# Performance work log

Measured on AMD Instinct MI355X. Metric: run time of the kernel, lower is better.

## Reference

```python
import jax, jax.numpy as jnp
import numpy as np

N = 80000      # points
H = 32         # neighbors per point
K = 15         # kernel points (torch-points3d default)
CIN = 128
COUT = 256
D2 = COUT // 4  # 64
INFL = 0.4      # point_influence = prev_grid_size * sigma
KP_RADIUS = 1.5 * INFL  # torch-points3d kernel radius
EPS = 1e-5
SLOPE = 0.2


def setup_inputs() -> dict:
    key = jax.random.key(0)
    ks = jax.random.split(key, 12)
    feats = jax.random.normal(ks[0], (N, CIN), jnp.float32)
    xyz = jax.random.uniform(ks[1], (N, 3), dtype=jnp.float32)
    batch = jnp.zeros((N,), jnp.int32)
    neighbor_idx = jax.random.randint(ks[2], (N, H), 0, N)
    # unary_1: Linear(CIN, D2, bias=False) + BN params
    W1 = jax.random.normal(ks[3], (CIN, D2), jnp.float32) / np.float32(np.sqrt(CIN))
    g1 = jnp.ones((D2,), jnp.float32); b1 = jnp.zeros((D2,), jnp.float32)
    # fixed kernel points inside ball of radius KP_RADIUS (buffer, not trained)
    kdir = jax.random.normal(ks[4], (K, 3), jnp.float32)
    kdir = kdir / jnp.linalg.norm(kdir, axis=1, keepdims=True)
    kp_points = kdir * jax.random.uniform(ks[5], (K, 1), dtype=jnp.float32) * KP_RADIUS
    # per-kernel-point weight matrices [K, D2, D2]
    kp_weights = jax.random.normal(ks[6], (K, D2, D2), jnp.float32) / np.float32(np.sqrt(K * D2))
    # unary_2: Linear(D2, COUT, bias=False) + BN params
    W2 = jax.random.normal(ks[7], (D2, COUT), jnp.float32) / np.float32(np.sqrt(D2))
    g2 = jnp.ones((COUT,), jnp.float32); b2 = jnp.zeros((COUT,), jnp.float32)
    # shortcut: Linear(CIN, COUT, bias=False) + BN params
    Wsc = jax.random.normal(ks[8], (CIN, COUT), jnp.float32) / np.float32(np.sqrt(CIN))
    gsc = jnp.ones((COUT,), jnp.float32); bsc = jnp.zeros((COUT,), jnp.float32)
    return {"feats": feats, "xyz": xyz, "batch": batch, "neighbor_idx": neighbor_idx,
            "W1": W1, "g1": g1, "b1": b1, "kp_points": kp_points, "kp_weights": kp_weights,
            "W2": W2, "g2": g2, "b2": b2, "Wsc": Wsc, "gsc": gsc, "bsc": bsc}


def _bn(x, g, b):
    # FastBatchNorm1d training-mode forward on [N, C]: biased batch stats
    m = jnp.mean(x, axis=0)
    v = jnp.var(x, axis=0)
    return (x - m) * jax.lax.rsqrt(v + EPS) * g + b


def _act(x):
    return jax.nn.leaky_relu(x, SLOPE)


def reference(feats, xyz, batch, neighbor_idx, W1, g1, b1, kp_points, kp_weights,
              W2, g2, b2, Wsc, gsc, bsc):
    # unary_1
    x = _act(_bn(feats @ W1, g1, b1))              # [N, D2]
    # KPConv: gather neighbors, kernel-point linear influence, weighted aggregation
    neighbors = xyz[neighbor_idx] - xyz[:, None, :]            # [N, H, 3]
    diff = neighbors[:, :, None, :] - kp_points[None, None]    # [N, H, K, 3]
    sq = jnp.sum(diff * diff, axis=-1)                          # [N, H, K]
    w = jnp.maximum(1.0 - jnp.sqrt(sq) / INFL, 0.0)             # linear influence
    nx = x[neighbor_idx]                                        # [N, H, D2]
    fk = jnp.einsum('nhk,nhd->nkd', w, nx)                      # [N, K, D2]
    x = jnp.einsum('nkd,kde->ne', fk, kp_weights)               # [N, D2]
    # unary_2
    x = _act(_bn(x @ W2, g2, b2))                               # [N, COUT]
    # shortcut (in_channels != out_channels -> Linear + BN)
    shortcut = _bn(feats @ Wsc, gsc, bsc)                       # [N, COUT]
    return x + shortcut
```

## Files before the change

kernel.cpp:

```cpp
#include <hip/hip_runtime.h>
#include <math.h>

#define NPTS 80000
#define NBH 32
#define KP 15
#define CIN 128
#define COUT 256
#define D2 64
#define INFL 0.4f
#define EPS 1e-5f
#define SLOPE 0.2f

typedef __attribute__((ext_vector_type(8))) short short8;
typedef __attribute__((ext_vector_type(4))) float f32x4;

__device__ inline ushort f2b(float x) {
  unsigned u = __float_as_uint(x);
  return (ushort)((u + 0x7FFFu + ((u >> 16) & 1u)) >> 16);
}
__device__ inline float b2f(ushort v) { return __uint_as_float(((unsigned)v) << 16); }

__global__ __launch_bounds__(256) void k_prep(const float* __restrict__ feats,
                                              const float* __restrict__ W1,
                                              const float* __restrict__ W2,
                                              const float* __restrict__ Wsc,
                                              const float* __restrict__ kw,
                                              ushort* __restrict__ featsb,
                                              ushort* __restrict__ w1s,
                                              ushort* __restrict__ w2s,
                                              ushort* __restrict__ wscs,
                                              ushort* __restrict__ kws) {
  const int NF4 = NPTS * CIN / 4;
  const int TOT = NF4 + 118784;
  int stride = gridDim.x * 256;
  for (int i = blockIdx.x * 256 + threadIdx.x; i < TOT; i += stride) {
    if (i < NF4) {
      float4 v = reinterpret_cast<const float4*>(feats)[i];
      ushort4 o;
      o.x = f2b(v.x); o.y = f2b(v.y); o.z = f2b(v.z); o.w = f2b(v.w);
      reinterpret_cast<ushort4*>(featsb)[i] = o;
    } else {
      int j = i - NF4;
      const float* src;
      ushort* dst;
      int logN;
      if (j < 8192)       { src = W1;  dst = w1s;  logN = 6; }
      else if (j < 24576) { j -= 8192;  src = W2;  dst = w2s;  logN = 8; }
      else if (j < 57344) { j -= 24576; src = Wsc; dst = wscs; logN = 8; }
      else                { j -= 57344; src = kw;  dst = kws;  logN = 6; }
      int N = 1 << logN, NT = N >> 4;
      int k = j >> logN, n = j & (N - 1);
      int dsti = ((k >> 5) * NT + (n >> 4)) * 512 + (n & 15) * 32 + ((k >> 3) & 3) * 8 + (k & 7);
      dst[dsti] = f2b(src[j]);
    }
  }
}

template <int NCOLS>
__global__ __launch_bounds__(256) void k_gemm_mfma(const ushort* __restrict__ A,
                                                   const ushort* __restrict__ Bsw,
                                                   ushort* __restrict__ Cb, int K) {
  constexpr int NT = NCOLS / 16;
  int tid = threadIdx.x;
  int wave = tid >> 6, lane = tid & 63;
  int nn = lane & 15, q = lane >> 4;
  int row0 = blockIdx.x * 64 + wave * 16;
  f32x4 acc[NT];
#pragma unroll
  for (int c = 0; c < NT; ++c) acc[c] = (f32x4){0.f, 0.f, 0.f, 0.f};
  const ushort* ap = A + (size_t)(row0 + nn) * K + q * 8;
  int nch = K >> 5;
  for (int ch = 0; ch < nch; ++ch) {
    short8 af = *reinterpret_cast<const short8*>(ap + (size_t)ch * 32);
    const ushort* bp = Bsw + (size_t)ch * NT * 512 + nn * 32 + q * 8;
#pragma unroll
    for (int c = 0; c < NT; ++c) {
      short8 bf = *reinterpret_cast<const short8*>(bp + c * 512);
      acc[c] = __builtin_amdgcn_mfma_f32_16x16x32_bf16(af, bf, acc[c], 0, 0, 0);
    }
  }
#pragma unroll
  for (int c = 0; c < NT; ++c)
#pragma unroll
    for (int r = 0; r < 4; ++r)
      Cb[(size_t)(row0 + q * 4 + r) * NCOLS + c * 16 + nn] = f2b(acc[c][r]);
}

__global__ __launch_bounds__(256) void k_colstats_b16(const ushort* __restrict__ X, int units,
                                                      int cols, float* __restrict__ sum,
                                                      float* __restrict__ sumsq) {
  __shared__ float ls[2048], ls2[2048];
  int tid = threadIdx.x;
  int stride = gridDim.x * 256;
  float s[8], s2[8];
#pragma unroll
  for (int k = 0; k < 8; ++k) { s[k] = 0.f; s2[k] = 0.f; }
  for (int i = blockIdx.x * 256 + tid; i < units; i += stride) {
    short8 v = reinterpret_cast<const short8*>(X)[i];
#pragma unroll
    for (int k = 0; k < 8; ++k) {
      float f = b2f((ushort)v[k]);
      s[k] += f;
      s2[k] += f * f;
    }
  }
#pragma unroll
  for (int k = 0; k < 8; ++k) { ls[tid * 8 + k] = s[k]; ls2[tid * 8 + k] = s2[k]; }
  __syncthreads();
  if (tid < cols) {
    int P = cols >> 3;
    float a = 0.f, a2 = 0.f;
    for (int t = (tid >> 3); t < 256; t += P) {
      a += ls[t * 8 + (tid & 7)];
      a2 += ls2[t * 8 + (tid & 7)];
    }
    atomicAdd(&sum[tid], a);
    atomicAdd(&sumsq[tid], a2);
  }
}

__global__ __launch_bounds__(256) void k_normb(const ushort* __restrict__ X,
                                               const float* __restrict__ sum,
                                               const float* __restrict__ sumsq,
                                               const float* __restrict__ g,
                                               const float* __restrict__ b,
                                               ushort* __restrict__ out) {
  __shared__ float sc[64], sh[64];
  int tid = threadIdx.x;
  if (tid < 64) {
    float m = sum[tid] * (1.0f / NPTS);
    float v = sumsq[tid] * (1.0f / NPTS) - m * m;
    float s = g[tid] * rsqrtf(v + EPS);
    sc[tid] = s;
    sh[tid] = b[tid] - m * s;
  }
  __syncthreads();
  const int units = NPTS * 8;
  int stride = gridDim.x * 256;
  for (int i = blockIdx.x * 256 + tid; i < units; i += stride) {
    short8 v = reinterpret_cast<const short8*>(X)[i];
    int cb = (i & 7) * 8;
    short8 o;
#pragma unroll
    for (int k = 0; k < 8; ++k) {
      float a = b2f((ushort)v[k]) * sc[cb + k] + sh[cb + k];
      a = a > 0.f ? a : SLOPE * a;
      o[k] = (short)f2b(a);
    }
    reinterpret_cast<short8*>(out)[i] = o;
  }
}

__global__ __launch_bounds__(256) void k_kpfused(const ushort* __restrict__ X1b,
                                                 const float* __restrict__ xyz,
                                                 const int* __restrict__ nidx,
                                                 const float* __restrict__ kpp,
                                                 const ushort* __restrict__ kws,
                                                 const ushort* __restrict__ w2s,
                                                 ushort* __restrict__ Y3b) {
  __shared__ ushort s_xT[4][64][32];
  __shared__ ushort s_fk[30 * 512];
  __shared__ ushort s_y2[2 * 512];
  int tid = threadIdx.x;
  int w = tid >> 6, lane = tid & 63;
  int q = lane >> 4, nn = lane & 15;
  int l8 = lane >> 3, c8 = lane & 7;
  int n_base = blockIdx.x * 16;

  int kidx = nn < 15 ? nn : 0;
  float kpx = kpp[kidx * 3 + 0], kpy = kpp[kidx * 3 + 1], kpz = kpp[kidx * 3 + 2];

  for (int p = 0; p < 4; ++p) {
    int n = n_base + w * 4 + p;
    int nb = 0;
    float rx = 0.f, ry = 0.f, rz = 0.f;
    if (lane < 32) {
      nb = nidx[n * NBH + lane];
      rx = xyz[nb * 3 + 0] - xyz[n * 3 + 0];
      ry = xyz[nb * 3 + 1] - xyz[n * 3 + 1];
      rz = xyz[nb * 3 + 2] - xyz[n * 3 + 2];
    }
    short8 af;
#pragma unroll
    for (int j = 0; j < 8; ++j) {
      int hh = q * 8 + j;
      float dx = __shfl(rx, hh) - kpx;
      float dy = __shfl(ry, hh) - kpy;
      float dz = __shfl(rz, hh) - kpz;
      float dist = sqrtf(dx * dx + dy * dy + dz * dz);
      float wv = fmaxf(1.0f - dist * (1.0f / INFL), 0.0f);
      if (nn == 15) wv = 0.f;
      af[j] = (short)f2b(wv);
    }
#pragma unroll
    for (int it = 0; it < 4; ++it) {
      int hh = it * 8 + l8;
      int nbh = __shfl(nb, hh);
      short8 v = *reinterpret_cast<const short8*>(X1b + (size_t)nbh * 64 + c8 * 8);
      int hcol = hh ^ ((c8 & 3) << 3);
#pragma unroll
      for (int u = 0; u < 8; ++u) s_xT[w][c8 * 8 + u][hcol] = (ushort)v[u];
    }
    f32x4 acc[4];
#pragma unroll
    for (int c = 0; c < 4; ++c) {
      int d = c * 16 + nn;
      int key = (d >> 3) & 3;
      short8 bf = *reinterpret_cast<const short8*>(&s_xT[w][d][(q ^ key) << 3]);
      acc[c] = __builtin_amdgcn_mfma_f32_16x16x32_bf16(af, bf, (f32x4){0.f, 0.f, 0.f, 0.f}, 0, 0, 0);
    }
    int m = w * 4 + p;
#pragma unroll
    for (int c = 0; c < 4; ++c) {
#pragma unroll
      for (int r = 0; r < 4; ++r) {
        int kpt = q * 4 + r;
        if (kpt < 15) {
          int kap = kpt * 64 + c * 16 + nn;
          int ch = kap >> 5, t = kap & 31;
          int tp = t ^ (((ch >> 3) & 3) << 3);
          s_fk[ch * 512 + m * 32 + tp] = f2b(acc[c][r]);
        }
      }
    }
  }
  __syncthreads();

  f32x4 acc2 = (f32x4){0.f, 0.f, 0.f, 0.f};
  for (int ch = 0; ch < 30; ++ch) {
    int key = (ch >> 3) & 3;
    short8 a = *reinterpret_cast<const short8*>(&s_fk[ch * 512 + nn * 32 + ((q ^ key) << 3)]);
    short8 b = *reinterpret_cast<const short8*>(kws + (size_t)ch * 2048 + w * 512 + nn * 32 + q * 8);
    acc2 = __builtin_amdgcn_mfma_f32_16x16x32_bf16(a, b, acc2, 0, 0, 0);
  }
  {
    int e = w * 16 + nn;
    int ch2 = e >> 5, t = e & 31;
#pragma unroll
    for (int r = 0; r < 4; ++r) {
      int mm = q * 4 + r;
      int tp = t ^ (((mm >> 2) & 3) << 3);
      s_y2[ch2 * 512 + mm * 32 + tp] = f2b(acc2[r]);
    }
  }
  __syncthreads();

  short8 a0, a1;
  {
    int key = (nn >> 2) & 3;
    a0 = *reinterpret_cast<const short8*>(&s_y2[0 * 512 + nn * 32 + ((q ^ key) << 3)]);
    a1 = *reinterpret_cast<const short8*>(&s_y2[1 * 512 + nn * 32 + ((q ^ key) << 3)]);
  }
#pragma unroll
  for (int t4 = 0; t4 < 4; ++t4) {
    int ct = w * 4 + t4;
    short8 b0 = *reinterpret_cast<const short8*>(w2s + (0 * 16 + ct) * 512 + nn * 32 + q * 8);
    short8 b1 = *reinterpret_cast<const short8*>(w2s + (1 * 16 + ct) * 512 + nn * 32 + q * 8);
    f32x4 a = __builtin_amdgcn_mfma_f32_16x16x32_bf16(a0, b0, (f32x4){0.f, 0.f, 0.f, 0.f}, 0, 0, 0);
    a = __builtin_amdgcn_mfma_f32_16x16x32_bf16(a1, b1, a, 0, 0, 0);
#pragma unroll
    for (int r = 0; r < 4; ++r)
      Y3b[(size_t)(n_base + q * 4 + r) * 256 + ct * 16 + nn] = f2b(a[r]);
  }
}

__global__ __launch_bounds__(256) void k_final(const ushort* __restrict__ Y3,
                                               const ushort* __restrict__ YSC,
                                               const float* __restrict__ s3,
                                               const float* __restrict__ ss3,
                                               const float* __restrict__ g2,
                                               const float* __restrict__ b2,
                                               const float* __restrict__ ssc,
                                               const float* __restrict__ sssc,
                                               const float* __restrict__ gsc,
                                               const float* __restrict__ bsc,
                                               float* __restrict__ out) {
  __shared__ float sc3[256], sh3[256], scc[256], shc[256];
  int tid = threadIdx.x;
  {
    float m = s3[tid] * (1.0f / NPTS);
    float v = ss3[tid] * (1.0f / NPTS) - m * m;
    float s = g2[tid] * rsqrtf(v + EPS);
    sc3[tid] = s;
    sh3[tid] = b2[tid] - m * s;
    m = ssc[tid] * (1.0f / NPTS);
    v = sssc[tid] * (1.0f / NPTS) - m * m;
    s = gsc[tid] * rsqrtf(v + EPS);
    scc[tid] = s;
    shc[tid] = bsc[tid] - m * s;
  }
  __syncthreads();
  const int units = NPTS * 32;
  int stride = gridDim.x * 256;
  for (int i = blockIdx.x * 256 + tid; i < units; i += stride) {
    short8 a = reinterpret_cast<const short8*>(Y3)[i];
    short8 b = reinterpret_cast<const short8*>(YSC)[i];
    int cb = (i & 31) * 8;
    float o[8];
#pragma unroll
    for (int k = 0; k < 8; ++k) {
      float x = b2f((ushort)a[k]) * sc3[cb + k] + sh3[cb + k];
      x = x > 0.f ? x : SLOPE * x;
      o[k] = x + b2f((ushort)b[k]) * scc[cb + k] + shc[cb + k];
    }
    float4* O4 = reinterpret_cast<float4*>(out + (size_t)i * 8);
    O4[0] = make_float4(o[0], o[1], o[2], o[3]);
    O4[1] = make_float4(o[4], o[5], o[6], o[7]);
  }
}

extern "C" void kernel_launch(void* const* d_in, const int* in_sizes, int n_in,
                              void* d_out, int out_size, void* d_ws, size_t ws_size,
                              hipStream_t stream) {
  const float* feats = (const float*)d_in[0];
  const float* xyz   = (const float*)d_in[1];
  const int* nidx    = (const int*)d_in[3];
  const float* W1    = (const float*)d_in[4];
  const float* g1    = (const float*)d_in[5];
  const float* b1    = (const float*)d_in[6];
  const float* kpp   = (const float*)d_in[7];
  const float* kw    = (const float*)d_in[8];
  const float* W2    = (const float*)d_in[9];
  const float* g2    = (const float*)d_in[10];
  const float* b2    = (const float*)d_in[11];
  const float* Wsc   = (const float*)d_in[12];
  const float* gsc   = (const float*)d_in[13];
  const float* bsc   = (const float*)d_in[14];
  float* out = (float*)d_out;

  char* ws = (char*)d_ws;
  ushort* featsb = (ushort*)ws;
  ushort* X1r    = (ushort*)(ws + 20480000);
  ushort* X1b    = (ushort*)(ws + 30720000);
  ushort* Y3b    = (ushort*)(ws + 40960000);
  ushort* YSCb   = (ushort*)(ws + 81920000);
  ushort* w1s    = (ushort*)(ws + 122880000);
  ushort* w2s    = w1s + 8192;
  ushort* wscs   = w2s + 16384;
  ushort* kws    = wscs + 32768;
  float*  ST     = (float*)(kws + 61440);
  float *S1 = ST, *SS1 = ST + 64;
  float *S3 = ST + 128, *SS3 = ST + 384;
  float *SSC = ST + 640, *SSSC = ST + 896;

  hipMemsetAsync(ST, 0, 1152 * sizeof(float), stream);
  k_prep<<<2048, 256, 0, stream>>>(feats, W1, W2, Wsc, kw, featsb, w1s, w2s, wscs, kws);
  k_gemm_mfma<64><<<1250, 256, 0, stream>>>(featsb, w1s, X1r, 128);
  k_colstats_b16<<<256, 256, 0, stream>>>(X1r, NPTS * 8, 64, S1, SS1);
  k_normb<<<512, 256, 0, stream>>>(X1r, S1, SS1, g1, b1, X1b);
  k_gemm_mfma<256><<<1250, 256, 0, stream>>>(featsb, wscs, YSCb, 128);
  k_colstats_b16<<<256, 256, 0, stream>>>(YSCb, NPTS * 32, 256, SSC, SSSC);
  k_kpfused<<<NPTS / 16, 256, 0, stream>>>(X1b, xyz, nidx, kpp, kws, w2s, Y3b);
  k_colstats_b16<<<256, 256, 0, stream>>>(Y3b, NPTS * 32, 256, S3, SS3);
  k_final<<<1024, 256, 0, stream>>>(Y3b, YSCb, S3, SS3, g2, b2, SSC, SSSC, gsc, bsc, out);
}
```

Before: 386.2 us.

## Fuse BN column stats into GEMM epilogues and precompute fp16 neighbor offsets

Removes the three separate column-statistics passes by reducing sums and sums of squares inside the GEMM and KPConv epilogues with shuffles and atomics. It also drops the bf16 copy of feats, converting fp32 rows to bf16 on the fly inside the GEMM. Neighbor relative positions are precomputed in k_prep as fp16 triples, and the gather into LDS is reorganized around pairs of neighbors with a new swizzle. The changes cut kernel launches and full-tensor rereads, at the cost of fp16 precision for offsets, more atomics, and an extra buffer of size N*H*3.

```diff
diff --git a/kernel.cpp b/kernel.cpp
--- a/kernel.cpp
+++ b/kernel.cpp
@@ -1,4 +1,5 @@
 #include <hip/hip_runtime.h>
+#include <hip/hip_fp16.h>
 #include <math.h>
 
 #define NPTS 80000
@@ -14,33 +15,48 @@
 typedef __attribute__((ext_vector_type(8))) short short8;
 typedef __attribute__((ext_vector_type(4))) float f32x4;
 
+union U8 { uint u[4]; short8 s; uint4 v; };
+
 __device__ inline ushort f2b(float x) {
   unsigned u = __float_as_uint(x);
   return (ushort)((u + 0x7FFFu + ((u >> 16) & 1u)) >> 16);
 }
 __device__ inline float b2f(ushort v) { return __uint_as_float(((unsigned)v) << 16); }
-
-__global__ __launch_bounds__(256) void k_prep(const float* __restrict__ feats,
+__device__ inline uint packbf(float a, float b) {
+  return (uint)f2b(a) | ((uint)f2b(b) << 16);
+}
+__device__ inline float h2f(ushort u) {
+  __half_raw r; r.x = u;
+  return __half2float(__half(r));
+}
+
+__global__ __launch_bounds__(256) void k_prep(const float* __restrict__ xyz,
+                                              const int* __restrict__ nidx,
                                               const float* __restrict__ W1,
                                               const float* __restrict__ W2,
                                               const float* __restrict__ Wsc,
                                               const float* __restrict__ kw,
-                                              ushort* __restrict__ featsb,
+                                              ushort* __restrict__ rdiff,
                                               ushort* __restrict__ w1s,
                                               ushort* __restrict__ w2s,
                                               ushort* __restrict__ wscs,
                                               ushort* __restrict__ kws) {
-  const int NF4 = NPTS * CIN / 4;
-  const int TOT = NF4 + 118784;
+  const int NPAIR = NPTS * NBH;
+  const int TOT = NPAIR + 118784;
   int stride = gridDim.x * 256;
   for (int i = blockIdx.x * 256 + threadIdx.x; i < TOT; i += stride) {
-    if (i < NF4) {
-      float4 v = reinterpret_cast<const float4*>(feats)[i];
-      ushort4 o;
-      o.x = f2b(v.x); o.y = f2b(v.y); o.z = f2b(v.z); o.w = f2b(v.w);
-      reinterpret_cast<ushort4*>(featsb)[i] = o;
+    if (i < NPAIR) {
+      int n = i >> 5;
+      int nb = nidx[i];
+      float rx = xyz[nb * 3 + 0] - xyz[n * 3 + 0];
+      float ry = xyz[nb * 3 + 1] - xyz[n * 3 + 1];
+      float rz = xyz[nb * 3 + 2] - xyz[n * 3 + 2];
+      __half hx = __float2half(rx), hy = __float2half(ry), hz = __float2half(rz);
+      rdiff[(size_t)i * 3 + 0] = __half_raw(hx).x;
+      rdiff[(size_t)i * 3 + 1] = __half_raw(hy).x;
+      rdiff[(size_t)i * 3 + 2] = __half_raw(hz).x;
     } else {
-      int j = i - NF4;
+      int j = i - NPAIR;
       const float* src;
       ushort* dst;
       int logN;
@@ -57,9 +73,11 @@
 }
 
 template <int NCOLS>
-__global__ __launch_bounds__(256) void k_gemm_mfma(const ushort* __restrict__ A,
+__global__ __launch_bounds__(256) void k_gemm_f32a(const float* __restrict__ A,
                                                    const ushort* __restrict__ Bsw,
-                                                   ushort* __restrict__ Cb, int K) {
+                                                   ushort* __restrict__ Cb, int K,
+                                                   float* __restrict__ S,
+                                                   float* __restrict__ SS) {
   constexpr int NT = NCOLS / 16;
   int tid = threadIdx.x;
   int wave = tid >> 6, lane = tid & 63;
@@ -68,54 +86,36 @@
   f32x4 acc[NT];
 #pragma unroll
   for (int c = 0; c < NT; ++c) acc[c] = (f32x4){0.f, 0.f, 0.f, 0.f};
-  const ushort* ap = A + (size_t)(row0 + nn) * K + q * 8;
+  const float* ap = A + (size_t)(row0 + nn) * K + q * 8;
   int nch = K >> 5;
   for (int ch = 0; ch < nch; ++ch) {
-    short8 af = *reinterpret_cast<const short8*>(ap + (size_t)ch * 32);
+    float4 f0 = *reinterpret_cast<const float4*>(ap + ch * 32);
+    float4 f1 = *reinterpret_cast<const float4*>(ap + ch * 32 + 4);
+    U8 af;
+    af.u[0] = packbf(f0.x, f0.y); af.u[1] = packbf(f0.z, f0.w);
+    af.u[2] = packbf(f1.x, f1.y); af.u[3] = packbf(f1.z, f1.w);
     const ushort* bp = Bsw + (size_t)ch * NT * 512 + nn * 32 + q * 8;
 #pragma unroll
     for (int c = 0; c < NT; ++c) {
-      short8 bf = *reinterpret_cast<const short8*>(bp + c * 512);
-      acc[c] = __builtin_amdgcn_mfma_f32_16x16x32_bf16(af, bf, acc[c], 0, 0, 0);
-    }
-  }
-#pragma unroll
-  for (int c = 0; c < NT; ++c)
-#pragma unroll
-    for (int r = 0; r < 4; ++r)
-      Cb[(size_t)(row0 + q * 4 + r) * NCOLS + c * 16 + nn] = f2b(acc[c][r]);
-}
-
-__global__ __launch_bounds__(256) void k_colstats_b16(const ushort* __restrict__ X, int units,
-                                                      int cols, float* __restrict__ sum,
-                                                      float* __restrict__ sumsq) {
-  __shared__ float ls[2048], ls2[2048];
-  int tid = threadIdx.x;
-  int stride = gridDim.x * 256;
-  float s[8], s2[8];
-#pragma unroll
-  for (int k = 0; k < 8; ++k) { s[k] = 0.f; s2[k] = 0.f; }
-  for (int i = blockIdx.x * 256 + tid; i < units; i += stride) {
-    short8 v = reinterpret_cast<const short8*>(X)[i];
-#pragma unroll
-    for (int k = 0; k < 8; ++k) {
-      float f = b2f((ushort)v[k]);
-      s[k] += f;
-      s2[k] += f * f;
-    }
-  }
-#pragma unroll
-  for (int k = 0; k < 8; ++k) { ls[tid * 8 + k] = s[k]; ls2[tid * 8 + k] = s2[k]; }
-  __syncthreads();
-  if (tid < cols) {
-    int P = cols >> 3;
-    float a = 0.f, a2 = 0.f;
-    for (int t = (tid >> 3); t < 256; t += P) {
-      a += ls[t * 8 + (tid & 7)];
-      a2 += ls2[t * 8 + (tid & 7)];
-    }
-    atomicAdd(&sum[tid], a);
-    atomicAdd(&sumsq[tid], a2);
+      U8 bf; bf.v = *reinterpret_cast<const uint4*>(bp + c * 512);
+      acc[c] = __builtin_amdgcn_mfma_f32_16x16x32_bf16(af.s, bf.s, acc[c], 0, 0, 0);
+    }
+  }
+#pragma unroll
+  for (int c = 0; c < NT; ++c) {
+    float s = 0.f, s2 = 0.f;
+#pragma unroll
+    for (int r = 0; r < 4; ++r) {
+      float v = acc[c][r];
+      s += v; s2 += v * v;
+      Cb[(size_t)(row0 + q * 4 + r) * NCOLS + c * 16 + nn] = f2b(v);
+    }
+    s += __shfl_xor(s, 16);  s += __shfl_xor(s, 32);
+    s2 += __shfl_xor(s2, 16); s2 += __shfl_xor(s2, 32);
+    if (q == 0) {
+      atomicAdd(&S[c * 16 + nn], s);
+      atomicAdd(&SS[c * 16 + nn], s2);
+    }
   }
 }
 
@@ -151,75 +151,82 @@
   }
 }
 
-__global__ __launch_bounds__(256) void k_kpfused(const ushort* __restrict__ X1b,
-                                                 const float* __restrict__ xyz,
-                                                 const int* __restrict__ nidx,
-                                                 const float* __restrict__ kpp,
-                                                 const ushort* __restrict__ kws,
-                                                 const ushort* __restrict__ w2s,
-                                                 ushort* __restrict__ Y3b) {
-  __shared__ ushort s_xT[4][64][32];
+__global__ __launch_bounds__(256, 3) void k_kpfused(const ushort* __restrict__ X1b,
+                                                    const ushort* __restrict__ rdiff,
+                                                    const int* __restrict__ nidx,
+                                                    const float* __restrict__ kpp,
+                                                    const ushort* __restrict__ kws,
+                                                    const ushort* __restrict__ w2s,
+                                                    ushort* __restrict__ Y3b,
+                                                    float* __restrict__ S3,
+                                                    float* __restrict__ SS3) {
+  __shared__ uint s_xi[4][1280];
   __shared__ ushort s_fk[30 * 512];
   __shared__ ushort s_y2[2 * 512];
   int tid = threadIdx.x;
   int w = tid >> 6, lane = tid & 63;
   int q = lane >> 4, nn = lane & 15;
-  int l8 = lane >> 3, c8 = lane & 7;
   int n_base = blockIdx.x * 16;
-
   int kidx = nn < 15 ? nn : 0;
   float kpx = kpp[kidx * 3 + 0], kpy = kpp[kidx * 3 + 1], kpz = kpp[kidx * 3 + 2];
+  uint* sx = s_xi[w];
 
   for (int p = 0; p < 4; ++p) {
     int n = n_base + w * 4 + p;
-    int nb = 0;
-    float rx = 0.f, ry = 0.f, rz = 0.f;
-    if (lane < 32) {
-      nb = nidx[n * NBH + lane];
-      rx = xyz[nb * 3 + 0] - xyz[n * 3 + 0];
-      ry = xyz[nb * 3 + 1] - xyz[n * 3 + 1];
-      rz = xyz[nb * 3 + 2] - xyz[n * 3 + 2];
-    }
-    short8 af;
+#pragma unroll
+    for (int i = 0; i < 4; ++i) {
+      int t = i * 4 + q;
+      int nb0 = nidx[n * NBH + 2 * t];
+      int nb1 = nidx[n * NBH + 2 * t + 1];
+      uint2 a = *reinterpret_cast<const uint2*>(X1b + (size_t)nb0 * 64 + nn * 4);
+      uint2 b = *reinterpret_cast<const uint2*>(X1b + (size_t)nb1 * 64 + nn * 4);
+      uint d0 = (a.x & 0xFFFFu) | (b.x << 16);
+      uint d1 = (a.x >> 16) | (b.x & 0xFFFF0000u);
+      uint d2 = (a.y & 0xFFFFu) | (b.y << 16);
+      uint d3 = (a.y >> 16) | (b.y & 0xFFFF0000u);
+      int tp = t ^ ((nn & 3) << 2);
+      sx[(nn * 4 + 0) * 20 + tp] = d0;
+      sx[(nn * 4 + 1) * 20 + tp] = d1;
+      sx[(nn * 4 + 2) * 20 + tp] = d2;
+      sx[(nn * 4 + 3) * 20 + tp] = d3;
+    }
+    const ushort* rp = rdiff + ((size_t)n * NBH + q * 8) * 3;
+    uint4 r0 = *reinterpret_cast<const uint4*>(rp);
+    uint4 r1 = *reinterpret_cast<const uint4*>(rp + 8);
+    uint4 r2 = *reinterpret_cast<const uint4*>(rp + 16);
+    uint wv[12] = {r0.x, r0.y, r0.z, r0.w, r1.x, r1.y, r1.z, r1.w, r2.x, r2.y, r2.z, r2.w};
+    float wgt[8];
 #pragma unroll
     for (int j = 0; j < 8; ++j) {
-      int hh = q * 8 + j;
-      float dx = __shfl(rx, hh) - kpx;
-      float dy = __shfl(ry, hh) - kpy;
-      float dz = __shfl(rz, hh) - kpz;
+      int i0 = 3 * j, i1 = 3 * j + 1, i2 = 3 * j + 2;
+      float rx = h2f((i0 & 1) ? (ushort)(wv[i0 >> 1] >> 16) : (ushort)(wv[i0 >> 1] & 0xFFFF));
+      float ry = h2f((i1 & 1) ? (ushort)(wv[i1 >> 1] >> 16) : (ushort)(wv[i1 >> 1] & 0xFFFF));
+      float rz = h2f((i2 & 1) ? (ushort)(wv[i2 >> 1] >> 16) : (ushort)(wv[i2 >> 1] & 0xFFFF));
+      float dx = rx - kpx, dy = ry - kpy, dz = rz - kpz;
       float dist = sqrtf(dx * dx + dy * dy + dz * dz);
-      float wv = fmaxf(1.0f - dist * (1.0f / INFL), 0.0f);
-      if (nn == 15) wv = 0.f;
-      af[j] = (short)f2b(wv);
-    }
-#pragma unroll
-    for (int it = 0; it < 4; ++it) {
-      int hh = it * 8 + l8;
-      int nbh = __shfl(nb, hh);
-      short8 v = *reinterpret_cast<const short8*>(X1b + (size_t)nbh * 64 + c8 * 8);
-      int hcol = hh ^ ((c8 & 3) << 3);
-#pragma unroll
-      for (int u = 0; u < 8; ++u) s_xT[w][c8 * 8 + u][hcol] = (ushort)v[u];
-    }
-    f32x4 acc[4];
+      float t = fmaxf(1.0f - dist * (1.0f / INFL), 0.0f);
+      wgt[j] = (nn == 15) ? 0.f : t;
+    }
+    U8 af;
+#pragma unroll
+    for (int j2 = 0; j2 < 4; ++j2) af.u[j2] = packbf(wgt[2 * j2], wgt[2 * j2 + 1]);
+    int m = w * 4 + p;
 #pragma unroll
     for (int c = 0; c < 4; ++c) {
       int d = c * 16 + nn;
-      int key = (d >> 3) & 3;
-      short8 bf = *reinterpret_cast<const short8*>(&s_xT[w][d][(q ^ key) << 3]);
-      acc[c] = __builtin_amdgcn_mfma_f32_16x16x32_bf16(af, bf, (f32x4){0.f, 0.f, 0.f, 0.f}, 0, 0, 0);
-    }
-    int m = w * 4 + p;
-#pragma unroll
-    for (int c = 0; c < 4; ++c) {
+      int db3 = nn >> 2;
+      U8 bf;
+      bf.v = *reinterpret_cast<const uint4*>(&sx[d * 20 + ((q ^ db3) << 2)]);
+      f32x4 acc = __builtin_amdgcn_mfma_f32_16x16x32_bf16(af.s, bf.s,
+                                                          (f32x4){0.f, 0.f, 0.f, 0.f}, 0, 0, 0);
 #pragma unroll
       for (int r = 0; r < 4; ++r) {
         int kpt = q * 4 + r;
         if (kpt < 15) {
-          int kap = kpt * 64 + c * 16 + nn;
-          int ch = kap >> 5, t = kap & 31;
-          int tp = t ^ (((ch >> 3) & 3) << 3);
-          s_fk[ch * 512 + m * 32 + tp] = f2b(acc[c][r]);
+          int kap = kpt * 64 + d;
+          int ch = kap >> 5, t2 = kap & 31;
+          int tp2 = t2 ^ (((ch >> 3) & 3) << 3);
+          s_fk[ch * 512 + m * 32 + tp2] = f2b(acc[r]);
         }
       }
     }
@@ -229,9 +236,10 @@
   f32x4 acc2 = (f32x4){0.f, 0.f, 0.f, 0.f};
   for (int ch = 0; ch < 30; ++ch) {
     int key = (ch >> 3) & 3;
-    short8 a = *reinterpret_cast<const short8*>(&s_fk[ch * 512 + nn * 32 + ((q ^ key) << 3)]);
-    short8 b = *reinterpret_cast<const short8*>(kws + (size_t)ch * 2048 + w * 512 + nn * 32 + q * 8);
-    acc2 = __builtin_amdgcn_mfma_f32_16x16x32_bf16(a, b, acc2, 0, 0, 0);
+    U8 a, b;
+    a.v = *reinterpret_cast<const uint4*>(&s_fk[ch * 512 + nn * 32 + ((q ^ key) << 3)]);
+    b.v = *reinterpret_cast<const uint4*>(kws + (size_t)ch * 2048 + w * 512 + nn * 32 + q * 8);
+    acc2 = __builtin_amdgcn_mfma_f32_16x16x32_bf16(a.s, b.s, acc2, 0, 0, 0);
   }
   {
     int e = w * 16 + nn;
@@ -245,19 +253,28 @@
   }
   __syncthreads();
 
-  short8 a0, a1;
+  U8 a0, a1;
   {
     int key = (nn >> 2) & 3;
-    a0 = *reinterpret_cast<const short8*>(&s_y2[0 * 512 + nn * 32 + ((q ^ key) << 3)]);
-    a1 = *reinterpret_cast<const short8*>(&s_y2[1 * 512 + nn * 32 + ((q ^ key) << 3)]);
+    a0.v = *reinterpret_cast<const uint4*>(&s_y2[0 * 512 + nn * 32 + ((q ^ key) << 3)]);
+    a1.v = *reinterpret_cast<const uint4*>(&s_y2[1 * 512 + nn * 32 + ((q ^ key) << 3)]);
   }
 #pragma unroll
   for (int t4 = 0; t4 < 4; ++t4) {
     int ct = w * 4 + t4;
-    short8 b0 = *reinterpret_cast<const short8*>(w2s + (0 * 16 + ct) * 512 + nn * 32 + q * 8);
-    short8 b1 = *reinterpret_cast<const short8*>(w2s + (1 * 16 + ct) * 512 + nn * 32 + q * 8);
-    f32x4 a = __builtin_amdgcn_mfma_f32_16x16x32_bf16(a0, b0, (f32x4){0.f, 0.f, 0.f, 0.f}, 0, 0, 0);
-    a = __builtin_amdgcn_mfma_f32_16x16x32_bf16(a1, b1, a, 0, 0, 0);
+    U8 b0, b1;
+    b0.v = *reinterpret_cast<const uint4*>(w2s + (0 * 16 + ct) * 512 + nn * 32 + q * 8);
+    b1.v = *reinterpret_cast<const uint4*>(w2s + (1 * 16 + ct) * 512 + nn * 32 + q * 8);
+    f32x4 a = __builtin_amdgcn_mfma_f32_16x16x32_bf16(a0.s, b0.s, (f32x4){0.f, 0.f, 0.f, 0.f}, 0, 0, 0);
+    a = __builtin_amdgcn_mfma_f32_16x16x32_bf16(a1.s, b1.s, a, 0, 0, 0);
+    float s = a[0] + a[1] + a[2] + a[3];
+    float s2 = a[0] * a[0] + a[1] * a[1] + a[2] * a[2] + a[3] * a[3];
+    s += __shfl_xor(s, 16);  s += __shfl_xor(s, 32);
+    s2 += __shfl_xor(s2, 16); s2 += __shfl_xor(s2, 32);
+    if (q == 0) {
+      atomicAdd(&S3[ct * 16 + nn], s);
+      atomicAdd(&SS3[ct * 16 + nn], s2);
+    }
 #pragma unroll
     for (int r = 0; r < 4; ++r)
       Y3b[(size_t)(n_base + q * 4 + r) * 256 + ct * 16 + nn] = f2b(a[r]);
@@ -329,28 +346,25 @@
   float* out = (float*)d_out;
 
   char* ws = (char*)d_ws;
-  ushort* featsb = (ushort*)ws;
-  ushort* X1r    = (ushort*)(ws + 20480000);
-  ushort* X1b    = (ushort*)(ws + 30720000);
-  ushort* Y3b    = (ushort*)(ws + 40960000);
-  ushort* YSCb   = (ushort*)(ws + 81920000);
-  ushort* w1s    = (ushort*)(ws + 122880000);
-  ushort* w2s    = w1s + 8192;
-  ushort* wscs   = w2s + 16384;
-  ushort* kws    = wscs + 32768;
-  float*  ST     = (float*)(kws + 61440);
+  ushort* X1r   = (ushort*)ws;
+  ushort* X1b   = (ushort*)(ws + 10240000);
+  ushort* Y3b   = (ushort*)(ws + 20480000);
+  ushort* YSCb  = (ushort*)(ws + 61440000);
+  ushort* rdiff = (ushort*)(ws + 102400000);
+  ushort* w1s   = (ushort*)(ws + 117760000);
+  ushort* w2s   = (ushort*)(ws + 117776384);
+  ushort* wscs  = (ushort*)(ws + 117809152);
+  ushort* kws   = (ushort*)(ws + 117874688);
+  float*  ST    = (float*)(ws + 117997568);
   float *S1 = ST, *SS1 = ST + 64;
   float *S3 = ST + 128, *SS3 = ST + 384;
   float *SSC = ST + 640, *SSSC = ST + 896;
 
   hipMemsetAsync(ST, 0, 1152 * sizeof(float), stream);
-  k_prep<<<2048, 256, 0, stream>>>(feats, W1, W2, Wsc, kw, featsb, w1s, w2s, wscs, kws);
-  k_gemm_mfma<64><<<1250, 256, 0, stream>>>(featsb, w1s, X1r, 128);
-  k_colstats_b16<<<256, 256, 0, stream>>>(X1r, NPTS * 8, 64, S1, SS1);
+  k_prep<<<4096, 256, 0, stream>>>(xyz, nidx, W1, W2, Wsc, kw, rdiff, w1s, w2s, wscs, kws);
+  k_gemm_f32a<64><<<1250, 256, 0, stream>>>(feats, w1s, X1r, 128, S1, SS1);
   k_normb<<<512, 256, 0, stream>>>(X1r, S1, SS1, g1, b1, X1b);
-  k_gemm_mfma<256><<<1250, 256, 0, stream>>>(featsb, wscs, YSCb, 128);
-  k_colstats_b16<<<256, 256, 0, stream>>>(YSCb, NPTS * 32, 256, SSC, SSSC);
-  k_kpfused<<<NPTS / 16, 256, 0, stream>>>(X1b, xyz, nidx, kpp, kws, w2s, Y3b);
-  k_colstats_b16<<<256, 256, 0, stream>>>(Y3b, NPTS * 32, 256, S3, SS3);
+  k_gemm_f32a<256><<<1250, 256, 0, stream>>>(feats, wscs, YSCb, 128, SSC, SSSC);
+  k_kpfused<<<NPTS / 16, 256, 0, stream>>>(X1b, rdiff, nidx, kpp, kws, w2s, Y3b, S3, SS3);
   k_final<<<1024, 256, 0, stream>>>(Y3b, YSCb, S3, SS3, g2, b2, SSC, SSSC, gsc, bsc, out);
 }
```

Measured after the change: 646.5 us. 1.67x slower.
